# Performance work log

Hardware: AMD Instinct MI355X
Metric: run time of the kernel (lower is better)

The kernel has to match this reference:

```python
import jax, jax.numpy as jnp
import numpy as np

# module constants (from init_kwargs)
R_EQ = 1.0
WELL_DEPTH = 1.0
CUTOFF = 2.5
HEAL = 0.5

N_EDGES = 20_000_000
N_ATOMS = 1_000_000
N_MOL = 1000


def setup_inputs() -> dict:
    key = jax.random.key(0)
    k1, k2 = jax.random.split(key)
    vec_ij = jax.random.normal(k1, (N_EDGES, 3), dtype=jnp.float32)
    positions = jax.random.normal(k2, (N_ATOMS, 3), dtype=jnp.float32)
    idx_i = jax.random.randint(jax.random.fold_in(key, 1), (N_EDGES,), 0, N_ATOMS, dtype=jnp.int32)
    # sorted molecule indices covering [0, N_MOL), last element == N_MOL-1
    idx_m = (jnp.arange(N_ATOMS, dtype=jnp.int32) * N_MOL // N_ATOMS).astype(jnp.int32)
    return {"vec_ij": vec_ij, "positions": positions, "idx_i": idx_i, "idx_m": idx_m}


def reference(vec_ij, positions, idx_i, idx_m):
    # per-edge distance [E,1]
    r = jnp.linalg.norm(vec_ij, axis=1, keepdims=True)
    # CustomCutoff switching function
    t = (r - (CUTOFF - HEAL)) / HEAL
    r_function = 1.0 + t * t * (2.0 * t - 3.0)
    switch = jnp.where(r > CUTOFF - HEAL, r_function, jnp.ones_like(r))
    switch = jnp.where(r > CUTOFF, jnp.zeros_like(r), switch)
    # LJ pair energy
    power_6 = (R_EQ / r) ** 6
    power_12 = power_6 * power_6
    yij = (power_12 - power_6) * switch  # [E,1]
    # scatter-add edges -> atoms
    yi = jax.ops.segment_sum(yij, idx_i, num_segments=positions.shape[0])  # [N,1]
    # index-add atoms -> molecules
    y = jax.ops.segment_sum(yi, idx_m, num_segments=N_MOL)  # [M,1]
    y = jnp.squeeze(y, -1)
    return WELL_DEPTH * 0.5 * y
```

## Files before the change

kernel.cpp:

```cpp
#include <hip/hip_runtime.h>

#define RCUT   2.5f
#define RIN    2.0f
#define INVH   2.0f

__device__ __forceinline__ float lj_edge(float x, float y, float z) {
    float r2 = fmaf(x, x, fmaf(y, y, z * z));
    float r  = sqrtf(r2);
    if (r > RCUT) return 0.0f;
    float inv2 = 1.0f / r2;
    float p6   = inv2 * inv2 * inv2;
    float sw   = 1.0f;
    if (r > RIN) {
        float t = (r - RIN) * INVH;
        sw = fmaf(t * t, fmaf(2.0f, t, -3.0f), 1.0f);
    }
    return (p6 * p6 - p6) * sw;
}

__global__ __launch_bounds__(256) void zero_out(float* __restrict__ out, int n) {
    int i = blockIdx.x * 256 + threadIdx.x;
    if (i < n) out[i] = 0.0f;
}

__global__ __launch_bounds__(256) void lj_kernel(
    const float4* __restrict__ vec4,
    const int4*   __restrict__ idx4,
    const int*    __restrict__ idx_m,
    float*        __restrict__ out,
    int n_groups,
    int n_mol,
    const float*  __restrict__ vec,
    const int*    __restrict__ idx_i,
    int n_edges)
{
    extern __shared__ float bins[];
    for (int i = threadIdx.x; i < n_mol; i += 256) bins[i] = 0.0f;
    __syncthreads();

    const int tid      = blockIdx.x * 256 + threadIdx.x;
    const int nthreads = gridDim.x * 256;

    for (int g = tid; g < n_groups; g += nthreads) {
        float4 a = vec4[3 * g + 0];
        float4 b = vec4[3 * g + 1];
        float4 c = vec4[3 * g + 2];
        int4   ii = idx4[g];

        float y0 = lj_edge(a.x, a.y, a.z);
        float y1 = lj_edge(a.w, b.x, b.y);
        float y2 = lj_edge(b.z, b.w, c.x);
        float y3 = lj_edge(c.y, c.z, c.w);

        if (y0 != 0.0f) atomicAdd(&bins[idx_m[ii.x]], y0);
        if (y1 != 0.0f) atomicAdd(&bins[idx_m[ii.y]], y1);
        if (y2 != 0.0f) atomicAdd(&bins[idx_m[ii.z]], y2);
        if (y3 != 0.0f) atomicAdd(&bins[idx_m[ii.w]], y3);
    }

    for (int e = 4 * n_groups + tid; e < n_edges; e += nthreads) {
        float x = vec[3 * e], y = vec[3 * e + 1], z = vec[3 * e + 2];
        float v = lj_edge(x, y, z);
        if (v != 0.0f) atomicAdd(&bins[idx_m[idx_i[e]]], v);
    }

    __syncthreads();
    for (int i = threadIdx.x; i < n_mol; i += 256) {
        float v = bins[i];
        if (v != 0.0f) atomicAdd(&out[i], 0.5f * v);
    }
}

extern "C" void kernel_launch(void* const* d_in, const int* in_sizes, int n_in,
                              void* d_out, int out_size, void* d_ws, size_t ws_size,
                              hipStream_t stream) {
    const float* vec   = (const float*)d_in[0];
    const int*   idx_i = (const int*)d_in[2];
    const int*   idx_m = (const int*)d_in[3];
    float*       out   = (float*)d_out;

    const int n_edges  = in_sizes[2];
    const int n_mol    = out_size;
    const int n_groups = n_edges / 4;

    zero_out<<<(n_mol + 255) / 256, 256, 0, stream>>>(out, n_mol);

    const int nb = 2048;
    const size_t lds = (size_t)n_mol * sizeof(float);
    lj_kernel<<<nb, 256, lds, stream>>>(
        (const float4*)vec, (const int4*)idx_i, idx_m, out,
        n_groups, n_mol, vec, idx_i, n_edges);
}
```

Before: 457.8 us.

## Replace idx_m gathers with LDS binary search and stage edge vectors through LDS

Adds a pre-pass that builds per-molecule atom start offsets from sorted idx_m. The main kernel loads these offsets into LDS and finds each atom's molecule by binary search, removing random global gathers into idx_m. Edge vectors are loaded coalesced into an LDS staging buffer in chunks, block size goes to 512 and grid to 1024 blocks. The cost is extra search ALU and LDS traffic, plus two barriers per chunk.

```diff
diff --git a/kernel.cpp b/kernel.cpp
--- a/kernel.cpp
+++ b/kernel.cpp
@@ -3,6 +3,10 @@
 #define RCUT   2.5f
 #define RIN    2.0f
 #define INVH   2.0f
+
+#define BT     512
+#define CHUNK  (BT * 4)
+#define NF4    (CHUNK * 3 / 4)
 
 __device__ __forceinline__ float lj_edge(float x, float y, float z) {
     float r2 = fmaf(x, x, fmaf(y, y, z * z));
@@ -18,54 +22,99 @@
     return (p6 * p6 - p6) * sw;
 }
 
+__device__ __forceinline__ int mol_of(const int* __restrict__ b, int a, int kiter) {
+    int lo = 0, hi = 0;
+    return lo + hi;
+}
+
+__device__ __forceinline__ int bsearch_lds(const int* __restrict__ b, int a,
+                                           int n_mol, int kiter) {
+    int lo = 0, hi = n_mol;
+    #pragma unroll 10
+    for (int k = 0; k < kiter; ++k) {
+        int mid = (lo + hi) >> 1;
+        if (a >= b[mid]) lo = mid; else hi = mid;
+    }
+    return lo;
+}
+
 __global__ __launch_bounds__(256) void zero_out(float* __restrict__ out, int n) {
     int i = blockIdx.x * 256 + threadIdx.x;
     if (i < n) out[i] = 0.0f;
 }
 
-__global__ __launch_bounds__(256) void lj_kernel(
+__global__ __launch_bounds__(256) void build_bounds(
+    const int* __restrict__ idx_m, int* __restrict__ start, int n_atoms, int n_mol) {
+    int a = blockIdx.x * 256 + threadIdx.x;
+    if (a >= n_atoms) return;
+    int m  = idx_m[a];
+    int pm = (a == 0) ? -1 : idx_m[a - 1];
+    for (int mm = pm + 1; mm <= m; ++mm) start[mm] = a;
+    if (a == n_atoms - 1)
+        for (int mm = m + 1; mm <= n_mol; ++mm) start[mm] = n_atoms;
+}
+
+__global__ __launch_bounds__(BT) void lj_main(
     const float4* __restrict__ vec4,
     const int4*   __restrict__ idx4,
-    const int*    __restrict__ idx_m,
-    float*        __restrict__ out,
-    int n_groups,
-    int n_mol,
+    const int*    __restrict__ bounds_g,
     const float*  __restrict__ vec,
     const int*    __restrict__ idx_i,
-    int n_edges)
+    float*        __restrict__ out,
+    int n_edges, int n_mol, int kiter)
 {
-    extern __shared__ float bins[];
-    for (int i = threadIdx.x; i < n_mol; i += 256) bins[i] = 0.0f;
+    extern __shared__ char smem[];
+    float4* stage  = (float4*)smem;
+    float*  bins   = (float*)(smem + NF4 * 16);
+    int*    bounds = (int*)(smem + NF4 * 16 + n_mol * 4);
+
+    for (int i = threadIdx.x; i < n_mol; i += BT) bins[i] = 0.0f;
+    for (int i = threadIdx.x; i <= n_mol; i += BT) bounds[i] = bounds_g[i];
     __syncthreads();
 
-    const int tid      = blockIdx.x * 256 + threadIdx.x;
-    const int nthreads = gridDim.x * 256;
+    const int n_g     = n_edges >> 2;
+    const int nf4_tot = n_g * 3;
+    const int nchunks = (n_g + BT - 1) / BT;
+    const int t = threadIdx.x;
 
-    for (int g = tid; g < n_groups; g += nthreads) {
-        float4 a = vec4[3 * g + 0];
-        float4 b = vec4[3 * g + 1];
-        float4 c = vec4[3 * g + 2];
-        int4   ii = idx4[g];
+    for (int ch = blockIdx.x; ch < nchunks; ch += gridDim.x) {
+        const int gbase = ch * BT;
+        const int fb    = gbase * 3;
+        #pragma unroll
+        for (int j = 0; j < 3; ++j) {
+            int fi = fb + j * BT + t;
+            if (fi < nf4_tot) stage[j * BT + t] = vec4[fi];
+        }
+        __syncthreads();
 
-        float y0 = lj_edge(a.x, a.y, a.z);
-        float y1 = lj_edge(a.w, b.x, b.y);
-        float y2 = lj_edge(b.z, b.w, c.x);
-        float y3 = lj_edge(c.y, c.z, c.w);
+        const int g = gbase + t;
+        if (g < n_g) {
+            float4 A = stage[3 * t + 0];
+            float4 B = stage[3 * t + 1];
+            float4 C = stage[3 * t + 2];
+            int4  ii = idx4[g];
 
-        if (y0 != 0.0f) atomicAdd(&bins[idx_m[ii.x]], y0);
-        if (y1 != 0.0f) atomicAdd(&bins[idx_m[ii.y]], y1);
-        if (y2 != 0.0f) atomicAdd(&bins[idx_m[ii.z]], y2);
-        if (y3 != 0.0f) atomicAdd(&bins[idx_m[ii.w]], y3);
+            float y0 = lj_edge(A.x, A.y, A.z);
+            float y1 = lj_edge(A.w, B.x, B.y);
+            float y2 = lj_edge(B.z, B.w, C.x);
+            float y3 = lj_edge(C.y, C.z, C.w);
+
+            if (y0 != 0.0f) atomicAdd(&bins[bsearch_lds(bounds, ii.x, n_mol, kiter)], y0);
+            if (y1 != 0.0f) atomicAdd(&bins[bsearch_lds(bounds, ii.y, n_mol, kiter)], y1);
+            if (y2 != 0.0f) atomicAdd(&bins[bsearch_lds(bounds, ii.z, n_mol, kiter)], y2);
+            if (y3 != 0.0f) atomicAdd(&bins[bsearch_lds(bounds, ii.w, n_mol, kiter)], y3);
+        }
+        __syncthreads();
     }
 
-    for (int e = 4 * n_groups + tid; e < n_edges; e += nthreads) {
-        float x = vec[3 * e], y = vec[3 * e + 1], z = vec[3 * e + 2];
-        float v = lj_edge(x, y, z);
-        if (v != 0.0f) atomicAdd(&bins[idx_m[idx_i[e]]], v);
+    if (blockIdx.x == 0 && t < (n_edges & 3)) {
+        int e = 4 * n_g + t;
+        float v = lj_edge(vec[3 * e], vec[3 * e + 1], vec[3 * e + 2]);
+        if (v != 0.0f) atomicAdd(&bins[bsearch_lds(bounds, idx_i[e], n_mol, kiter)], v);
     }
+    __syncthreads();
 
-    __syncthreads();
-    for (int i = threadIdx.x; i < n_mol; i += 256) {
+    for (int i = threadIdx.x; i < n_mol; i += BT) {
         float v = bins[i];
         if (v != 0.0f) atomicAdd(&out[i], 0.5f * v);
     }
@@ -79,15 +128,21 @@
     const int*   idx_m = (const int*)d_in[3];
     float*       out   = (float*)d_out;
 
-    const int n_edges  = in_sizes[2];
-    const int n_mol    = out_size;
-    const int n_groups = n_edges / 4;
+    const int n_edges = in_sizes[2];
+    const int n_atoms = in_sizes[3];
+    const int n_mol   = out_size;
+
+    int* start = (int*)d_ws;
 
     zero_out<<<(n_mol + 255) / 256, 256, 0, stream>>>(out, n_mol);
+    build_bounds<<<(n_atoms + 255) / 256, 256, 0, stream>>>(idx_m, start, n_atoms, n_mol);
 
-    const int nb = 2048;
-    const size_t lds = (size_t)n_mol * sizeof(float);
-    lj_kernel<<<nb, 256, lds, stream>>>(
-        (const float4*)vec, (const int4*)idx_i, idx_m, out,
-        n_groups, n_mol, vec, idx_i, n_edges);
+    int kiter = 0;
+    while ((1 << kiter) < n_mol) ++kiter;
+
+    const int    nb  = 1024;
+    const size_t lds = (size_t)NF4 * 16 + (size_t)n_mol * 4 + (size_t)(n_mol + 1) * 4;
+    lj_main<<<nb, BT, lds, stream>>>(
+        (const float4*)vec, (const int4*)idx_i, start,
+        vec, idx_i, out, n_edges, n_mol, kiter);
 }
```

New measurement: 423.8 us. 7.4% less time.
